# Optimization experiments

Measured on AMD Instinct MI355X. Metric: run time of the kernel, lower is better.

Reference implementation:

```python
import jax, jax.numpy as jnp
import numpy as np
from jax import lax

THRESH_WIDTH = 20  # default thresh_width in soft_skeletonize
SMOOTH = 1.0


def _max_pool3(x):
    # 3x3 max pool, stride 1, padding 1 (torch pads with -inf for max pool)
    return lax.reduce_window(x, -jnp.inf, lax.max,
                             (1, 1, 3, 3), (1, 1, 1, 1),
                             [(0, 0), (0, 0), (1, 1), (1, 1)])


def _soft_skeletonize(x):
    def body(i, x):
        min_pool_x = -_max_pool3(-x)
        contour = jax.nn.relu(_max_pool3(min_pool_x) - min_pool_x)
        return jax.nn.relu(x - contour)
    return lax.fori_loop(0, THRESH_WIDTH, body, x)


def _norm_intersection(center_line, vessel):
    clf = center_line.ravel()
    vf = vessel.ravel()
    intersection = jnp.sum(clf * vf)
    return (intersection + SMOOTH) / (jnp.sum(clf) + SMOOTH)


def setup_inputs() -> dict:
    key = jax.random.key(0)
    k1, k2 = jax.random.split(key)
    shape = (16, 1, 1024, 1024)
    pred = jax.random.uniform(k1, shape, dtype=jnp.float32)
    gt = jax.random.uniform(k2, shape, dtype=jnp.float32)
    return {"pred": pred, "gt": gt}


def reference(pred, gt):
    # channel == 1 path: pred used as-is (float)
    pred = pred.astype(jnp.float32)
    cl_pred = _soft_skeletonize(pred)
    target_skeleton = _soft_skeletonize(gt)
    iflat = _norm_intersection(cl_pred, gt)
    tflat = _norm_intersection(target_skeleton, pred)
    intersection = iflat * tflat
    loss = 1.0 - 2.0 * intersection / (iflat + tflat)
    return loss  # scalar; .squeeze() in torch is a no-op here
```

## Files before the change

kernel.cpp:

```cpp
#include <hip/hip_runtime.h>
#include <math.h>


#define IMG_H 1024
#define IMG_W 1024
#define IMG_N (IMG_H * IMG_W)
#define NIMG  16
#define NZ    32
#define BH    32
#define NBANDS (IMG_H / BH)
#define K     4
#define EW    258
#define NBLK  (NZ * NBANDS)
#define ITER_PAIRS ((BH + 6 * K) / 2)

typedef _Float16 h2 __attribute__((ext_vector_type(2)));

__device__ __forceinline__ h2 hmin2(h2 a, h2 b) { return __builtin_elementwise_min(a, b); }
__device__ __forceinline__ h2 hmax2(h2 a, h2 b) { return __builtin_elementwise_max(a, b); }

union U32H { unsigned u; h2 h; };
__device__ __forceinline__ unsigned as_u(h2 h) { U32H t; t.h = h; return t.u; }
__device__ __forceinline__ h2 as_h2(unsigned u) { U32H t; t.u = u; return t.h; }

struct Hp { h2 lo, hi; };
struct St { Hp hm1, hm2, m2, m3, q1, q2, x1, x2, x3, xc; };

template<int BUF>
__device__ __forceinline__ Hp stage_step(
    St& s, h2 rmask, int t, const uint2 (&e2)[2][EW])
{
    h2 lp = as_h2(e2[BUF][t].y);
    h2 rp = as_h2(e2[BUF][t + 2].x);
    h2 midx = (h2){s.xc.lo[1], s.xc.hi[0]};
    h2 hlo = hmin2(hmin2((h2){lp[0], s.xc.lo[0]}, s.xc.lo), midx);
    h2 hhi = hmin2(hmin2(midx, s.xc.hi), (h2){s.xc.hi[1], rp[0]});
    h2 mlo = hmin2(hmin2(hmin2(s.hm1.lo, s.hm2.lo), hlo), rmask);
    h2 mhi = hmin2(hmin2(hmin2(s.hm1.hi, s.hm2.hi), hhi), rmask);
    h2 midm = (h2){s.m2.lo[1], s.m2.hi[0]};
    h2 qlo = hmax2(hmax2((h2){lp[1], s.m2.lo[0]}, s.m2.lo), midm);
    h2 qhi = hmax2(hmax2(midm, s.m2.hi), (h2){s.m2.hi[1], rp[1]});
    h2 Mlo = hmax2(hmax2(s.q1.lo, s.q2.lo), qlo);
    h2 Mhi = hmax2(hmax2(s.q1.hi, s.q2.hi), qhi);
    const h2 Z2 = (h2){(_Float16)0.f, (_Float16)0.f};
    h2 elo = hmax2(s.x3.lo - hmax2(Mlo - s.m3.lo, Z2), Z2);
    h2 ehi = hmax2(s.x3.hi - hmax2(Mhi - s.m3.hi, Z2), Z2);
    s.hm1 = s.hm2; s.hm2.lo = hlo; s.hm2.hi = hhi;
    s.m3  = s.m2;  s.m2.lo  = mlo; s.m2.hi  = mhi;
    s.q1  = s.q2;  s.q2.lo  = qlo; s.q2.hi  = qhi;
    s.x3  = s.x2;  s.x2 = s.x1;    s.x1 = s.xc;
    Hp e; e.lo = elo; e.hi = ehi;
    return e;
}

template<int BUF, int FIRST, int LAST>
__device__ __forceinline__ void iter_step(
    int y, int t, int c, int r0, St (&st)[K],
    const float* __restrict__ f32src, const unsigned short* __restrict__ bsrc,
    unsigned short* __restrict__ bdst, const float* __restrict__ oth,
    float& a1, float& a2, uint2 (&e2)[K][2][EW])
{
    const _Float16 HINF = (_Float16)__builtin_huge_valf();
    const h2 PINF2 = (h2){HINF, HINF};
    const h2 NINF2 = (h2){-HINF, -HINF};

    Hp xnext; xnext.lo = PINF2; xnext.hi = PINF2;
    if ((unsigned)(y + 1) < (unsigned)IMG_H) {
        if constexpr (FIRST) {
            float4 f = *(const float4*)(f32src + (size_t)(y + 1) * IMG_W + c);
            xnext.lo = (h2){(_Float16)f.x, (_Float16)f.y};
            xnext.hi = (h2){(_Float16)f.z, (_Float16)f.w};
        } else {
            uint2 u = *(const uint2*)(bsrc + (size_t)(y + 1) * IMG_W + c);
            xnext.lo = as_h2(u.x);
            xnext.hi = as_h2(u.y);
        }
    }
    __syncthreads();

    h2 rm = ((unsigned)(y - 13) < (unsigned)IMG_H) ? PINF2 : NINF2;
    Hp eK = stage_step<BUF>(st[K - 1], rm, t, e2[K - 1]);
    #pragma unroll
    for (int k = K - 2; k >= 0; --k) {
        rm = ((unsigned)(y - 4 * k - 1) < (unsigned)IMG_H) ? PINF2 : NINF2;
        Hp e = stage_step<BUF>(st[k], rm, t, e2[k]);
        h2 em = ((unsigned)(y - 4 * k - 3) < (unsigned)IMG_H) ? NINF2 : PINF2;
        st[k + 1].xc.lo = hmax2(e.lo, em);
        st[k + 1].xc.hi = hmax2(e.hi, em);
    }
    st[0].xc = xnext;

    #pragma unroll
    for (int k = 0; k < K; ++k) {
        e2[k][BUF ^ 1][t + 1] = make_uint2(
            as_u((h2){st[k].xc.lo[0], st[k].m2.lo[0]}),
            as_u((h2){st[k].xc.hi[1], st[k].m2.hi[1]}));
    }

    int orow = y - (4 * (K - 1) + 3);
    if ((unsigned)(orow - r0) < (unsigned)BH) {
        if constexpr (!LAST) {
            *(uint2*)(bdst + (size_t)orow * IMG_W + c) =
                make_uint2(as_u(eK.lo), as_u(eK.hi));
        } else {
            float4 ov = *(const float4*)(oth + (size_t)orow * IMG_W + c);
            float e0 = (float)eK.lo[0], e1 = (float)eK.lo[1];
            float e2f = (float)eK.hi[0], e3 = (float)eK.hi[1];
            a1 += e0 * ov.x + e1 * ov.y + e2f * ov.z + e3 * ov.w;
            a2 += e0 + e1 + e2f + e3;
        }
    }
}

template<int FIRST, int LAST>
__global__ __launch_bounds__(256, 2) void skel(
    const unsigned short* __restrict__ src, unsigned short* __restrict__ dst,
    const float* __restrict__ pred32, const float* __restrict__ gt32,
    double* __restrict__ partials)
{
    __shared__ uint2 e2[K][2][EW];
    __shared__ double l1[4], l2[4];

    const int t = threadIdx.x, c = 4 * t;
    const int band = blockIdx.x, z = blockIdx.y;
    const int r0 = band * BH;
    const _Float16 HINF = (_Float16)__builtin_huge_valf();
    const h2 PINF2 = (h2){HINF, HINF};
    const h2 NINF2 = (h2){-HINF, -HINF};

    const float* f32src = (z < NIMG) ? pred32 + (size_t)z * IMG_N
                                     : gt32 + (size_t)(z - NIMG) * IMG_N;
    const unsigned short* bsrc = FIRST ? nullptr : src + (size_t)z * IMG_N;
    unsigned short* bdst = LAST ? nullptr : dst + (size_t)z * IMG_N;
    const float* oth = LAST ? ((z < NIMG) ? gt32 + (size_t)z * IMG_N
                                          : pred32 + (size_t)(z - NIMG) * IMG_N)
                            : nullptr;

    if (t < K) {
        #pragma unroll
        for (int b = 0; b < 2; ++b) {
            e2[t][b][0]      = make_uint2(0u, 0xFC007C00u);
            e2[t][b][EW - 1] = make_uint2(0xFC007C00u, 0u);
        }
    }

    St st[K];
    #pragma unroll
    for (int k = 0; k < K; ++k) {
        st[k].hm1.lo = st[k].hm1.hi = PINF2;
        st[k].hm2.lo = st[k].hm2.hi = PINF2;
        st[k].m2.lo  = st[k].m2.hi  = NINF2;
        st[k].m3.lo  = st[k].m3.hi  = NINF2;
        st[k].q1.lo  = st[k].q1.hi  = NINF2;
        st[k].q2.lo  = st[k].q2.hi  = NINF2;
        st[k].x1.lo  = st[k].x1.hi  = PINF2;
        st[k].x2.lo  = st[k].x2.hi  = PINF2;
        st[k].x3.lo  = st[k].x3.hi  = PINF2;
        st[k].xc.lo  = st[k].xc.hi  = PINF2;
    }

    const int y0 = r0 - 2 * K;
    if ((unsigned)y0 < (unsigned)IMG_H) {
        if constexpr (FIRST) {
            float4 f = *(const float4*)(f32src + (size_t)y0 * IMG_W + c);
            st[0].xc.lo = (h2){(_Float16)f.x, (_Float16)f.y};
            st[0].xc.hi = (h2){(_Float16)f.z, (_Float16)f.w};
        } else {
            uint2 u = *(const uint2*)(bsrc + (size_t)y0 * IMG_W + c);
            st[0].xc.lo = as_h2(u.x);
            st[0].xc.hi = as_h2(u.y);
        }
    }

    #pragma unroll
    for (int k = 0; k < K; ++k) {
        e2[k][0][t + 1] = make_uint2(
            as_u((h2){st[k].xc.lo[0], st[k].m2.lo[0]}),
            as_u((h2){st[k].xc.hi[1], st[k].m2.hi[1]}));
    }

    float a1 = 0.f, a2 = 0.f;
    for (int p = 0; p < ITER_PAIRS; ++p) {
        int y = y0 + 2 * p;
        iter_step<0, FIRST, LAST>(y,     t, c, r0, st, f32src, bsrc, bdst, oth, a1, a2, e2);
        iter_step<1, FIRST, LAST>(y + 1, t, c, r0, st, f32src, bsrc, bdst, oth, a1, a2, e2);
    }

    if constexpr (LAST) {
        double d1 = a1, d2 = a2;
        for (int off = 32; off; off >>= 1) {
            d1 += __shfl_down(d1, off);
            d2 += __shfl_down(d2, off);
        }
        const int w = t >> 6;
        if ((t & 63) == 0) { l1[w] = d1; l2[w] = d2; }
        __syncthreads();
        if (t == 0) {
            int bid = z * NBANDS + band;
            partials[2 * bid]     = l1[0] + l1[1] + l1[2] + l1[3];
            partials[2 * bid + 1] = l2[0] + l2[1] + l2[2] + l2[3];
        }
    }
}

__global__ __launch_bounds__(256) void finalize(
    const double* __restrict__ pp, float* __restrict__ out)
{
    __shared__ double sh[4][4];
    double i1 = 0, i2 = 0, t1 = 0, t2 = 0;
    for (int i = threadIdx.x; i < NBLK; i += 256) {
        double a = pp[2 * i], b = pp[2 * i + 1];
        if (i < NIMG * NBANDS) { i1 += a; i2 += b; }
        else                   { t1 += a; t2 += b; }
    }
    for (int off = 32; off; off >>= 1) {
        i1 += __shfl_down(i1, off); i2 += __shfl_down(i2, off);
        t1 += __shfl_down(t1, off); t2 += __shfl_down(t2, off);
    }
    const int w = threadIdx.x >> 6;
    if ((threadIdx.x & 63) == 0) { sh[0][w] = i1; sh[1][w] = i2; sh[2][w] = t1; sh[3][w] = t2; }
    __syncthreads();
    if (threadIdx.x == 0) {
        double s1 = 0, s2 = 0, s3 = 0, s4 = 0;
        for (int j = 0; j < 4; ++j) { s1 += sh[0][j]; s2 += sh[1][j]; s3 += sh[2][j]; s4 += sh[3][j]; }
        double iflat = (s1 + 1.0) / (s2 + 1.0);
        double tflat = (s3 + 1.0) / (s4 + 1.0);
        out[0] = (float)(1.0 - 2.0 * (iflat * tflat) / (iflat + tflat));
    }
}

extern "C" void kernel_launch(void* const* d_in, const int* in_sizes, int n_in,
                              void* d_out, int out_size, void* d_ws, size_t ws_size,
                              hipStream_t stream)
{
    const float* pred = (const float*)d_in[0];
    const float* gt   = (const float*)d_in[1];

    unsigned short* A = (unsigned short*)d_ws;
    unsigned short* B = A + (size_t)NZ * IMG_N;
    double* partials  = (double*)d_ws;
    dim3 grid(NBANDS, NZ);

    skel<1, 0><<<grid, 256, 0, stream>>>(nullptr, A, pred, gt, nullptr);
    skel<0, 0><<<grid, 256, 0, stream>>>(A, B, pred, gt, nullptr);
    skel<0, 0><<<grid, 256, 0, stream>>>(B, A, pred, gt, nullptr);
    skel<0, 0><<<grid, 256, 0, stream>>>(A, B, pred, gt, nullptr);
    skel<0, 1><<<grid, 256, 0, stream>>>(B, nullptr, pred, gt, partials);

    finalize<<<1, 256, 0, stream>>>(partials, (float*)d_out);
}
```

Baseline: 644.0 us.

## Fuse five skeleton iterations per pass and specialize interior bands without masks

```diff
diff --git a/kernel.cpp b/kernel.cpp
--- a/kernel.cpp
+++ b/kernel.cpp
@@ -9,7 +9,7 @@
 #define NZ    32
 #define BH    32
 #define NBANDS (IMG_H / BH)
-#define K     4
+#define K     5
 #define EW    258
 #define NBLK  (NZ * NBANDS)
 #define ITER_PAIRS ((BH + 6 * K) / 2)
@@ -23,20 +23,26 @@
 __device__ __forceinline__ unsigned as_u(h2 h) { U32H t; t.h = h; return t.u; }
 __device__ __forceinline__ h2 as_h2(unsigned u) { U32H t; t.u = u; return t.h; }
 
+#define HINF  ((_Float16)__builtin_huge_valf())
+#define PINF2 ((h2){HINF, HINF})
+#define NINF2 ((h2){-HINF, -HINF})
+
 struct Hp { h2 lo, hi; };
 struct St { Hp hm1, hm2, m2, m3, q1, q2, x1, x2, x3, xc; };
 
-template<int BUF>
+template<int BUF, bool MASK>
 __device__ __forceinline__ Hp stage_step(
-    St& s, h2 rmask, int t, const uint2 (&e2)[2][EW])
-{
-    h2 lp = as_h2(e2[BUF][t].y);
-    h2 rp = as_h2(e2[BUF][t + 2].x);
+    St& s, h2 rmask, int t,
+    const unsigned (&eX)[2][EW], const unsigned (&eY)[2][EW])
+{
+    h2 lp = as_h2(eY[BUF][t]);
+    h2 rp = as_h2(eX[BUF][t + 2]);
     h2 midx = (h2){s.xc.lo[1], s.xc.hi[0]};
     h2 hlo = hmin2(hmin2((h2){lp[0], s.xc.lo[0]}, s.xc.lo), midx);
     h2 hhi = hmin2(hmin2(midx, s.xc.hi), (h2){s.xc.hi[1], rp[0]});
-    h2 mlo = hmin2(hmin2(hmin2(s.hm1.lo, s.hm2.lo), hlo), rmask);
-    h2 mhi = hmin2(hmin2(hmin2(s.hm1.hi, s.hm2.hi), hhi), rmask);
+    h2 mlo = hmin2(hmin2(s.hm1.lo, s.hm2.lo), hlo);
+    h2 mhi = hmin2(hmin2(s.hm1.hi, s.hm2.hi), hhi);
+    if constexpr (MASK) { mlo = hmin2(mlo, rmask); mhi = hmin2(mhi, rmask); }
     h2 midm = (h2){s.m2.lo[1], s.m2.hi[0]};
     h2 qlo = hmax2(hmax2((h2){lp[1], s.m2.lo[0]}, s.m2.lo), midm);
     h2 qhi = hmax2(hmax2(midm, s.m2.hi), (h2){s.m2.hi[1], rp[1]});
@@ -53,48 +59,62 @@
     return e;
 }
 
-template<int BUF, int FIRST, int LAST>
+template<int BUF, bool MASK, int FIRST, int LAST>
 __device__ __forceinline__ void iter_step(
     int y, int t, int c, int r0, St (&st)[K],
     const float* __restrict__ f32src, const unsigned short* __restrict__ bsrc,
     unsigned short* __restrict__ bdst, const float* __restrict__ oth,
-    float& a1, float& a2, uint2 (&e2)[K][2][EW])
-{
-    const _Float16 HINF = (_Float16)__builtin_huge_valf();
-    const h2 PINF2 = (h2){HINF, HINF};
-    const h2 NINF2 = (h2){-HINF, -HINF};
-
-    Hp xnext; xnext.lo = PINF2; xnext.hi = PINF2;
-    if ((unsigned)(y + 1) < (unsigned)IMG_H) {
+    float& a1, float& a2,
+    unsigned (&eX)[K][2][EW], unsigned (&eY)[K][2][EW])
+{
+    Hp xnext;
+    if constexpr (MASK) {
+        xnext.lo = PINF2; xnext.hi = PINF2;
+        if ((unsigned)(y + 1) < (unsigned)IMG_H) {
+            if constexpr (FIRST) {
+                float4 f = *(const float4*)(f32src + (size_t)(y + 1) * IMG_W + c);
+                xnext.lo = (h2){(_Float16)f.x, (_Float16)f.y};
+                xnext.hi = (h2){(_Float16)f.z, (_Float16)f.w};
+            } else {
+                uint2 u = *(const uint2*)(bsrc + (size_t)(y + 1) * IMG_W + c);
+                xnext.lo = as_h2(u.x); xnext.hi = as_h2(u.y);
+            }
+        }
+    } else {
         if constexpr (FIRST) {
             float4 f = *(const float4*)(f32src + (size_t)(y + 1) * IMG_W + c);
             xnext.lo = (h2){(_Float16)f.x, (_Float16)f.y};
             xnext.hi = (h2){(_Float16)f.z, (_Float16)f.w};
         } else {
             uint2 u = *(const uint2*)(bsrc + (size_t)(y + 1) * IMG_W + c);
-            xnext.lo = as_h2(u.x);
-            xnext.hi = as_h2(u.y);
+            xnext.lo = as_h2(u.x); xnext.hi = as_h2(u.y);
         }
     }
     __syncthreads();
 
-    h2 rm = ((unsigned)(y - 13) < (unsigned)IMG_H) ? PINF2 : NINF2;
-    Hp eK = stage_step<BUF>(st[K - 1], rm, t, e2[K - 1]);
+    h2 rm = PINF2;
+    if constexpr (MASK)
+        rm = ((unsigned)(y - 4 * (K - 1) - 1) < (unsigned)IMG_H) ? PINF2 : NINF2;
+    Hp eK = stage_step<BUF, MASK>(st[K - 1], rm, t, eX[K - 1], eY[K - 1]);
     #pragma unroll
     for (int k = K - 2; k >= 0; --k) {
-        rm = ((unsigned)(y - 4 * k - 1) < (unsigned)IMG_H) ? PINF2 : NINF2;
-        Hp e = stage_step<BUF>(st[k], rm, t, e2[k]);
-        h2 em = ((unsigned)(y - 4 * k - 3) < (unsigned)IMG_H) ? NINF2 : PINF2;
-        st[k + 1].xc.lo = hmax2(e.lo, em);
-        st[k + 1].xc.hi = hmax2(e.hi, em);
+        if constexpr (MASK)
+            rm = ((unsigned)(y - 4 * k - 1) < (unsigned)IMG_H) ? PINF2 : NINF2;
+        Hp e = stage_step<BUF, MASK>(st[k], rm, t, eX[k], eY[k]);
+        if constexpr (MASK) {
+            h2 em = ((unsigned)(y - 4 * k - 3) < (unsigned)IMG_H) ? NINF2 : PINF2;
+            st[k + 1].xc.lo = hmax2(e.lo, em);
+            st[k + 1].xc.hi = hmax2(e.hi, em);
+        } else {
+            st[k + 1].xc = e;
+        }
     }
     st[0].xc = xnext;
 
     #pragma unroll
     for (int k = 0; k < K; ++k) {
-        e2[k][BUF ^ 1][t + 1] = make_uint2(
-            as_u((h2){st[k].xc.lo[0], st[k].m2.lo[0]}),
-            as_u((h2){st[k].xc.hi[1], st[k].m2.hi[1]}));
+        eX[k][BUF ^ 1][t + 1] = as_u((h2){st[k].xc.lo[0], st[k].m2.lo[0]});
+        eY[k][BUF ^ 1][t + 1] = as_u((h2){st[k].xc.hi[1], st[k].m2.hi[1]});
     }
 
     int orow = y - (4 * (K - 1) + 3);
@@ -112,21 +132,34 @@
     }
 }
 
+template<bool MASK, int FIRST, int LAST>
+__device__ __forceinline__ void run_band(
+    int y0, int t, int c, int r0, St (&st)[K],
+    const float* __restrict__ f32src, const unsigned short* __restrict__ bsrc,
+    unsigned short* __restrict__ bdst, const float* __restrict__ oth,
+    float& a1, float& a2,
+    unsigned (&eX)[K][2][EW], unsigned (&eY)[K][2][EW])
+{
+    for (int p = 0; p < ITER_PAIRS; ++p) {
+        int y = y0 + 2 * p;
+        iter_step<0, MASK, FIRST, LAST>(y,     t, c, r0, st, f32src, bsrc, bdst, oth, a1, a2, eX, eY);
+        iter_step<1, MASK, FIRST, LAST>(y + 1, t, c, r0, st, f32src, bsrc, bdst, oth, a1, a2, eX, eY);
+    }
+}
+
 template<int FIRST, int LAST>
 __global__ __launch_bounds__(256, 2) void skel(
     const unsigned short* __restrict__ src, unsigned short* __restrict__ dst,
     const float* __restrict__ pred32, const float* __restrict__ gt32,
     double* __restrict__ partials)
 {
-    __shared__ uint2 e2[K][2][EW];
+    __shared__ unsigned eX[K][2][EW];
+    __shared__ unsigned eY[K][2][EW];
     __shared__ double l1[4], l2[4];
 
     const int t = threadIdx.x, c = 4 * t;
     const int band = blockIdx.x, z = blockIdx.y;
     const int r0 = band * BH;
-    const _Float16 HINF = (_Float16)__builtin_huge_valf();
-    const h2 PINF2 = (h2){HINF, HINF};
-    const h2 NINF2 = (h2){-HINF, -HINF};
 
     const float* f32src = (z < NIMG) ? pred32 + (size_t)z * IMG_N
                                      : gt32 + (size_t)(z - NIMG) * IMG_N;
@@ -139,8 +172,8 @@
     if (t < K) {
         #pragma unroll
         for (int b = 0; b < 2; ++b) {
-            e2[t][b][0]      = make_uint2(0u, 0xFC007C00u);
-            e2[t][b][EW - 1] = make_uint2(0xFC007C00u, 0u);
+            eY[t][b][0]      = 0xFC007C00u;
+            eX[t][b][EW - 1] = 0xFC007C00u;
         }
     }
 
@@ -167,24 +200,21 @@
             st[0].xc.hi = (h2){(_Float16)f.z, (_Float16)f.w};
         } else {
             uint2 u = *(const uint2*)(bsrc + (size_t)y0 * IMG_W + c);
-            st[0].xc.lo = as_h2(u.x);
-            st[0].xc.hi = as_h2(u.y);
+            st[0].xc.lo = as_h2(u.x); st[0].xc.hi = as_h2(u.y);
         }
     }
 
     #pragma unroll
     for (int k = 0; k < K; ++k) {
-        e2[k][0][t + 1] = make_uint2(
-            as_u((h2){st[k].xc.lo[0], st[k].m2.lo[0]}),
-            as_u((h2){st[k].xc.hi[1], st[k].m2.hi[1]}));
+        eX[k][0][t + 1] = as_u((h2){st[k].xc.lo[0], st[k].m2.lo[0]});
+        eY[k][0][t + 1] = as_u((h2){st[k].xc.hi[1], st[k].m2.hi[1]});
     }
 
     float a1 = 0.f, a2 = 0.f;
-    for (int p = 0; p < ITER_PAIRS; ++p) {
-        int y = y0 + 2 * p;
-        iter_step<0, FIRST, LAST>(y,     t, c, r0, st, f32src, bsrc, bdst, oth, a1, a2, e2);
-        iter_step<1, FIRST, LAST>(y + 1, t, c, r0, st, f32src, bsrc, bdst, oth, a1, a2, e2);
-    }
+    if (band >= 1 && band <= NBANDS - 2)
+        run_band<false, FIRST, LAST>(y0, t, c, r0, st, f32src, bsrc, bdst, oth, a1, a2, eX, eY);
+    else
+        run_band<true,  FIRST, LAST>(y0, t, c, r0, st, f32src, bsrc, bdst, oth, a1, a2, eX, eY);
 
     if constexpr (LAST) {
         double d1 = a1, d2 = a2;
@@ -238,14 +268,13 @@
 
     unsigned short* A = (unsigned short*)d_ws;
     unsigned short* B = A + (size_t)NZ * IMG_N;
-    double* partials  = (double*)d_ws;
+    double* partials  = (double*)B;
     dim3 grid(NBANDS, NZ);
 
     skel<1, 0><<<grid, 256, 0, stream>>>(nullptr, A, pred, gt, nullptr);
     skel<0, 0><<<grid, 256, 0, stream>>>(A, B, pred, gt, nullptr);
     skel<0, 0><<<grid, 256, 0, stream>>>(B, A, pred, gt, nullptr);
-    skel<0, 0><<<grid, 256, 0, stream>>>(A, B, pred, gt, nullptr);
-    skel<0, 1><<<grid, 256, 0, stream>>>(B, nullptr, pred, gt, partials);
+    skel<0, 1><<<grid, 256, 0, stream>>>(A, nullptr, pred, gt, partials);
 
     finalize<<<1, 256, 0, stream>>>(partials, (float*)d_out);
 }
```

After: 711.2 us. +10.4%, slower.

## Process two rows per pipeline step to halve barriers and share vertical windows

Applied to the files above, without the earlier changes.

```diff
diff --git a/kernel.cpp b/kernel.cpp
--- a/kernel.cpp
+++ b/kernel.cpp
@@ -12,7 +12,7 @@
 #define K     4
 #define EW    258
 #define NBLK  (NZ * NBANDS)
-#define ITER_PAIRS ((BH + 6 * K) / 2)
+#define NPAIR 16
 
 typedef _Float16 h2 __attribute__((ext_vector_type(2)));
 
@@ -23,34 +23,64 @@
 __device__ __forceinline__ unsigned as_u(h2 h) { U32H t; t.h = h; return t.u; }
 __device__ __forceinline__ h2 as_h2(unsigned u) { U32H t; t.u = u; return t.h; }
 
+#define PXP 0x7C007C00u
+#define NXP 0xFC00FC00u
+#define HINF  ((_Float16)__builtin_huge_valf())
+#define PINF2 ((h2){HINF, HINF})
+#define NINF2 ((h2){-HINF, -HINF})
+
 struct Hp { h2 lo, hi; };
-struct St { Hp hm1, hm2, m2, m3, q1, q2, x1, x2, x3, xc; };
+
+struct St { Hp hm1, hm2, mpa, mpb, mppb, qpa, qpb, xpa, xpb, xppa, xppb, xca, xcb; };
 
 template<int BUF>
-__device__ __forceinline__ Hp stage_step(
-    St& s, h2 rmask, int t, const uint2 (&e2)[2][EW])
-{
-    h2 lp = as_h2(e2[BUF][t].y);
-    h2 rp = as_h2(e2[BUF][t + 2].x);
-    h2 midx = (h2){s.xc.lo[1], s.xc.hi[0]};
-    h2 hlo = hmin2(hmin2((h2){lp[0], s.xc.lo[0]}, s.xc.lo), midx);
-    h2 hhi = hmin2(hmin2(midx, s.xc.hi), (h2){s.xc.hi[1], rp[0]});
-    h2 mlo = hmin2(hmin2(hmin2(s.hm1.lo, s.hm2.lo), hlo), rmask);
-    h2 mhi = hmin2(hmin2(hmin2(s.hm1.hi, s.hm2.hi), hhi), rmask);
-    h2 midm = (h2){s.m2.lo[1], s.m2.hi[0]};
-    h2 qlo = hmax2(hmax2((h2){lp[1], s.m2.lo[0]}, s.m2.lo), midm);
-    h2 qhi = hmax2(hmax2(midm, s.m2.hi), (h2){s.m2.hi[1], rp[1]});
-    h2 Mlo = hmax2(hmax2(s.q1.lo, s.q2.lo), qlo);
-    h2 Mhi = hmax2(hmax2(s.q1.hi, s.q2.hi), qhi);
+__device__ __forceinline__ void stage_step(
+    St& s, int ya, int t,
+    const uint2 (&eXk)[2][EW], const uint2 (&eYk)[2][EW],
+    Hp& ea, Hp& eb)
+{
     const h2 Z2 = (h2){(_Float16)0.f, (_Float16)0.f};
-    h2 elo = hmax2(s.x3.lo - hmax2(Mlo - s.m3.lo, Z2), Z2);
-    h2 ehi = hmax2(s.x3.hi - hmax2(Mhi - s.m3.hi, Z2), Z2);
-    s.hm1 = s.hm2; s.hm2.lo = hlo; s.hm2.hi = hhi;
-    s.m3  = s.m2;  s.m2.lo  = mlo; s.m2.hi  = mhi;
-    s.q1  = s.q2;  s.q2.lo  = qlo; s.q2.hi  = qhi;
-    s.x3  = s.x2;  s.x2 = s.x1;    s.x1 = s.xc;
-    Hp e; e.lo = elo; e.hi = ehi;
-    return e;
+    uint2 lp = eYk[BUF][t];
+    uint2 rp = eXk[BUF][t + 2];
+    h2 lpx = as_h2(lp.x), lpm = as_h2(lp.y);
+    h2 rpx = as_h2(rp.x), rpm = as_h2(rp.y);
+
+    h2 midA = (h2){s.xca.lo[1], s.xca.hi[0]};
+    h2 haLo = hmin2(hmin2((h2){lpx[0], s.xca.lo[0]}, s.xca.lo), midA);
+    h2 haHi = hmin2(hmin2(midA, s.xca.hi), (h2){s.xca.hi[1], rpx[0]});
+    h2 midB = (h2){s.xcb.lo[1], s.xcb.hi[0]};
+    h2 hbLo = hmin2(hmin2((h2){lpx[1], s.xcb.lo[0]}, s.xcb.lo), midB);
+    h2 hbHi = hmin2(hmin2(midB, s.xcb.hi), (h2){s.xcb.hi[1], rpx[1]});
+
+    h2 rmA = as_h2(((unsigned)(ya - 1) < (unsigned)IMG_H) ? PXP : NXP);
+    h2 rmB = as_h2(((unsigned)(ya)     < (unsigned)IMG_H) ? PXP : NXP);
+    h2 maLo = hmin2(hmin2(hmin2(s.hm1.lo, s.hm2.lo), haLo), rmA);
+    h2 maHi = hmin2(hmin2(hmin2(s.hm1.hi, s.hm2.hi), haHi), rmA);
+    h2 mbLo = hmin2(hmin2(hmin2(s.hm2.lo, haLo), hbLo), rmB);
+    h2 mbHi = hmin2(hmin2(hmin2(s.hm2.hi, haHi), hbHi), rmB);
+
+    h2 midQa = (h2){s.mpa.lo[1], s.mpa.hi[0]};
+    h2 qaLo = hmax2(hmax2((h2){lpm[0], s.mpa.lo[0]}, s.mpa.lo), midQa);
+    h2 qaHi = hmax2(hmax2(midQa, s.mpa.hi), (h2){s.mpa.hi[1], rpm[0]});
+    h2 midQb = (h2){s.mpb.lo[1], s.mpb.hi[0]};
+    h2 qbLo = hmax2(hmax2((h2){lpm[1], s.mpb.lo[0]}, s.mpb.lo), midQb);
+    h2 qbHi = hmax2(hmax2(midQb, s.mpb.hi), (h2){s.mpb.hi[1], rpm[1]});
+
+    h2 MaLo = hmax2(hmax2(s.qpa.lo, s.qpb.lo), qaLo);
+    h2 MaHi = hmax2(hmax2(s.qpa.hi, s.qpb.hi), qaHi);
+    h2 MbLo = hmax2(hmax2(s.qpb.lo, qaLo), qbLo);
+    h2 MbHi = hmax2(hmax2(s.qpb.hi, qaHi), qbHi);
+
+    ea.lo = hmax2(s.xppa.lo - hmax2(MaLo - s.mppb.lo, Z2), Z2);
+    ea.hi = hmax2(s.xppa.hi - hmax2(MaHi - s.mppb.hi, Z2), Z2);
+    eb.lo = hmax2(s.xppb.lo - hmax2(MbLo - s.mpa.lo, Z2), Z2);
+    eb.hi = hmax2(s.xppb.hi - hmax2(MbHi - s.mpa.hi, Z2), Z2);
+
+    s.hm1.lo = haLo; s.hm1.hi = haHi; s.hm2.lo = hbLo; s.hm2.hi = hbHi;
+    s.mppb = s.mpb;
+    s.mpa.lo = maLo; s.mpa.hi = maHi; s.mpb.lo = mbLo; s.mpb.hi = mbHi;
+    s.qpa.lo = qaLo; s.qpa.hi = qaHi; s.qpb.lo = qbLo; s.qpb.hi = qbHi;
+    s.xppa = s.xpa; s.xppb = s.xpb; s.xpa = s.xca; s.xpb = s.xcb;
 }
 
 template<int BUF, int FIRST, int LAST>
@@ -58,57 +88,78 @@
     int y, int t, int c, int r0, St (&st)[K],
     const float* __restrict__ f32src, const unsigned short* __restrict__ bsrc,
     unsigned short* __restrict__ bdst, const float* __restrict__ oth,
-    float& a1, float& a2, uint2 (&e2)[K][2][EW])
-{
-    const _Float16 HINF = (_Float16)__builtin_huge_valf();
-    const h2 PINF2 = (h2){HINF, HINF};
-    const h2 NINF2 = (h2){-HINF, -HINF};
-
-    Hp xnext; xnext.lo = PINF2; xnext.hi = PINF2;
-    if ((unsigned)(y + 1) < (unsigned)IMG_H) {
-        if constexpr (FIRST) {
-            float4 f = *(const float4*)(f32src + (size_t)(y + 1) * IMG_W + c);
-            xnext.lo = (h2){(_Float16)f.x, (_Float16)f.y};
-            xnext.hi = (h2){(_Float16)f.z, (_Float16)f.w};
+    float& a1, float& a2,
+    uint2 (&eX)[K][2][EW], uint2 (&eY)[K][2][EW])
+{
+    int la = y + 2; la = la < 0 ? 0 : (la > IMG_H - 1 ? IMG_H - 1 : la);
+    int lb = y + 3; lb = lb < 0 ? 0 : (lb > IMG_H - 1 ? IMG_H - 1 : lb);
+    h2 gA = as_h2(((unsigned)(y + 2) < (unsigned)IMG_H) ? NXP : PXP);
+    h2 gB = as_h2(((unsigned)(y + 3) < (unsigned)IMG_H) ? NXP : PXP);
+    Hp xna, xnb;
+    if constexpr (FIRST) {
+        float4 fa = *(const float4*)(f32src + (size_t)la * IMG_W + c);
+        float4 fb = *(const float4*)(f32src + (size_t)lb * IMG_W + c);
+        xna.lo = (h2){(_Float16)fa.x, (_Float16)fa.y};
+        xna.hi = (h2){(_Float16)fa.z, (_Float16)fa.w};
+        xnb.lo = (h2){(_Float16)fb.x, (_Float16)fb.y};
+        xnb.hi = (h2){(_Float16)fb.z, (_Float16)fb.w};
+    } else {
+        uint2 ua = *(const uint2*)(bsrc + (size_t)la * IMG_W + c);
+        uint2 ub = *(const uint2*)(bsrc + (size_t)lb * IMG_W + c);
+        xna.lo = as_h2(ua.x); xna.hi = as_h2(ua.y);
+        xnb.lo = as_h2(ub.x); xnb.hi = as_h2(ub.y);
+    }
+    xna.lo = hmax2(xna.lo, gA); xna.hi = hmax2(xna.hi, gA);
+    xnb.lo = hmax2(xnb.lo, gB); xnb.hi = hmax2(xnb.hi, gB);
+
+    __syncthreads();
+
+    Hp ea, eb;
+    stage_step<BUF>(st[K - 1], y - 6 * (K - 1), t, eX[K - 1], eY[K - 1], ea, eb);
+    int orow = y - 6 * (K - 1) - 4;
+    if ((unsigned)(orow - r0) < (unsigned)BH) {
+        if constexpr (!LAST) {
+            *(uint2*)(bdst + (size_t)orow * IMG_W + c) = make_uint2(as_u(ea.lo), as_u(ea.hi));
         } else {
-            uint2 u = *(const uint2*)(bsrc + (size_t)(y + 1) * IMG_W + c);
-            xnext.lo = as_h2(u.x);
-            xnext.hi = as_h2(u.y);
-        }
-    }
-    __syncthreads();
-
-    h2 rm = ((unsigned)(y - 13) < (unsigned)IMG_H) ? PINF2 : NINF2;
-    Hp eK = stage_step<BUF>(st[K - 1], rm, t, e2[K - 1]);
+            float4 ov = *(const float4*)(oth + (size_t)orow * IMG_W + c);
+            float e0 = (float)ea.lo[0], e1 = (float)ea.lo[1];
+            float e2 = (float)ea.hi[0], e3 = (float)ea.hi[1];
+            a1 += e0 * ov.x + e1 * ov.y + e2 * ov.z + e3 * ov.w;
+            a2 += e0 + e1 + e2 + e3;
+        }
+    }
+    if ((unsigned)(orow + 1 - r0) < (unsigned)BH) {
+        if constexpr (!LAST) {
+            *(uint2*)(bdst + (size_t)(orow + 1) * IMG_W + c) = make_uint2(as_u(eb.lo), as_u(eb.hi));
+        } else {
+            float4 ov = *(const float4*)(oth + (size_t)(orow + 1) * IMG_W + c);
+            float e0 = (float)eb.lo[0], e1 = (float)eb.lo[1];
+            float e2 = (float)eb.hi[0], e3 = (float)eb.hi[1];
+            a1 += e0 * ov.x + e1 * ov.y + e2 * ov.z + e3 * ov.w;
+            a2 += e0 + e1 + e2 + e3;
+        }
+    }
+
     #pragma unroll
     for (int k = K - 2; k >= 0; --k) {
-        rm = ((unsigned)(y - 4 * k - 1) < (unsigned)IMG_H) ? PINF2 : NINF2;
-        Hp e = stage_step<BUF>(st[k], rm, t, e2[k]);
-        h2 em = ((unsigned)(y - 4 * k - 3) < (unsigned)IMG_H) ? NINF2 : PINF2;
-        st[k + 1].xc.lo = hmax2(e.lo, em);
-        st[k + 1].xc.hi = hmax2(e.hi, em);
-    }
-    st[0].xc = xnext;
+        Hp fa, fb;
+        int ya = y - 6 * k;
+        stage_step<BUF>(st[k], ya, t, eX[k], eY[k], fa, fb);
+        h2 eA = as_h2(((unsigned)(ya - 4) < (unsigned)IMG_H) ? NXP : PXP);
+        h2 eB = as_h2(((unsigned)(ya - 3) < (unsigned)IMG_H) ? NXP : PXP);
+        st[k + 1].xca.lo = hmax2(fa.lo, eA); st[k + 1].xca.hi = hmax2(fa.hi, eA);
+        st[k + 1].xcb.lo = hmax2(fb.lo, eB); st[k + 1].xcb.hi = hmax2(fb.hi, eB);
+    }
+    st[0].xca = xna; st[0].xcb = xnb;
 
     #pragma unroll
     for (int k = 0; k < K; ++k) {
-        e2[k][BUF ^ 1][t + 1] = make_uint2(
-            as_u((h2){st[k].xc.lo[0], st[k].m2.lo[0]}),
-            as_u((h2){st[k].xc.hi[1], st[k].m2.hi[1]}));
-    }
-
-    int orow = y - (4 * (K - 1) + 3);
-    if ((unsigned)(orow - r0) < (unsigned)BH) {
-        if constexpr (!LAST) {
-            *(uint2*)(bdst + (size_t)orow * IMG_W + c) =
-                make_uint2(as_u(eK.lo), as_u(eK.hi));
-        } else {
-            float4 ov = *(const float4*)(oth + (size_t)orow * IMG_W + c);
-            float e0 = (float)eK.lo[0], e1 = (float)eK.lo[1];
-            float e2f = (float)eK.hi[0], e3 = (float)eK.hi[1];
-            a1 += e0 * ov.x + e1 * ov.y + e2f * ov.z + e3 * ov.w;
-            a2 += e0 + e1 + e2f + e3;
-        }
+        eX[k][BUF ^ 1][t + 1] = make_uint2(
+            as_u((h2){st[k].xca.lo[0], st[k].xcb.lo[0]}),
+            as_u((h2){st[k].mpa.lo[0], st[k].mpb.lo[0]}));
+        eY[k][BUF ^ 1][t + 1] = make_uint2(
+            as_u((h2){st[k].xca.hi[1], st[k].xcb.hi[1]}),
+            as_u((h2){st[k].mpa.hi[1], st[k].mpb.hi[1]}));
     }
 }
 
@@ -118,15 +169,13 @@
     const float* __restrict__ pred32, const float* __restrict__ gt32,
     double* __restrict__ partials)
 {
-    __shared__ uint2 e2[K][2][EW];
+    __shared__ uint2 eX[K][2][EW];
+    __shared__ uint2 eY[K][2][EW];
     __shared__ double l1[4], l2[4];
 
     const int t = threadIdx.x, c = 4 * t;
     const int band = blockIdx.x, z = blockIdx.y;
     const int r0 = band * BH;
-    const _Float16 HINF = (_Float16)__builtin_huge_valf();
-    const h2 PINF2 = (h2){HINF, HINF};
-    const h2 NINF2 = (h2){-HINF, -HINF};
 
     const float* f32src = (z < NIMG) ? pred32 + (size_t)z * IMG_N
                                      : gt32 + (size_t)(z - NIMG) * IMG_N;
@@ -139,8 +188,8 @@
     if (t < K) {
         #pragma unroll
         for (int b = 0; b < 2; ++b) {
-            e2[t][b][0]      = make_uint2(0u, 0xFC007C00u);
-            e2[t][b][EW - 1] = make_uint2(0xFC007C00u, 0u);
+            eY[t][b][0]      = make_uint2(PXP, NXP);
+            eX[t][b][EW - 1] = make_uint2(PXP, NXP);
         }
     }
 
@@ -149,41 +198,57 @@
     for (int k = 0; k < K; ++k) {
         st[k].hm1.lo = st[k].hm1.hi = PINF2;
         st[k].hm2.lo = st[k].hm2.hi = PINF2;
-        st[k].m2.lo  = st[k].m2.hi  = NINF2;
-        st[k].m3.lo  = st[k].m3.hi  = NINF2;
-        st[k].q1.lo  = st[k].q1.hi  = NINF2;
-        st[k].q2.lo  = st[k].q2.hi  = NINF2;
-        st[k].x1.lo  = st[k].x1.hi  = PINF2;
-        st[k].x2.lo  = st[k].x2.hi  = PINF2;
-        st[k].x3.lo  = st[k].x3.hi  = PINF2;
-        st[k].xc.lo  = st[k].xc.hi  = PINF2;
-    }
-
-    const int y0 = r0 - 2 * K;
-    if ((unsigned)y0 < (unsigned)IMG_H) {
+        st[k].mpa.lo = st[k].mpa.hi = NINF2;
+        st[k].mpb.lo = st[k].mpb.hi = NINF2;
+        st[k].mppb.lo = st[k].mppb.hi = NINF2;
+        st[k].qpa.lo = st[k].qpa.hi = NINF2;
+        st[k].qpb.lo = st[k].qpb.hi = NINF2;
+        st[k].xpa.lo = st[k].xpa.hi = PINF2;
+        st[k].xpb.lo = st[k].xpb.hi = PINF2;
+        st[k].xppa.lo = st[k].xppa.hi = PINF2;
+        st[k].xppb.lo = st[k].xppb.hi = PINF2;
+        st[k].xca.lo = st[k].xca.hi = PINF2;
+        st[k].xcb.lo = st[k].xcb.hi = PINF2;
+    }
+
+    const int y0 = r0 - 8;
+    {
+        int la = y0 < 0 ? 0 : y0;
+        int lb = y0 + 1 < 0 ? 0 : y0 + 1;
+        h2 gA = as_h2(((unsigned)y0 < (unsigned)IMG_H) ? NXP : PXP);
+        h2 gB = as_h2(((unsigned)(y0 + 1) < (unsigned)IMG_H) ? NXP : PXP);
         if constexpr (FIRST) {
-            float4 f = *(const float4*)(f32src + (size_t)y0 * IMG_W + c);
-            st[0].xc.lo = (h2){(_Float16)f.x, (_Float16)f.y};
-            st[0].xc.hi = (h2){(_Float16)f.z, (_Float16)f.w};
+            float4 fa = *(const float4*)(f32src + (size_t)la * IMG_W + c);
+            float4 fb = *(const float4*)(f32src + (size_t)lb * IMG_W + c);
+            st[0].xca.lo = hmax2((h2){(_Float16)fa.x, (_Float16)fa.y}, gA);
+            st[0].xca.hi = hmax2((h2){(_Float16)fa.z, (_Float16)fa.w}, gA);
+            st[0].xcb.lo = hmax2((h2){(_Float16)fb.x, (_Float16)fb.y}, gB);
+            st[0].xcb.hi = hmax2((h2){(_Float16)fb.z, (_Float16)fb.w}, gB);
         } else {
-            uint2 u = *(const uint2*)(bsrc + (size_t)y0 * IMG_W + c);
-            st[0].xc.lo = as_h2(u.x);
-            st[0].xc.hi = as_h2(u.y);
+            uint2 ua = *(const uint2*)(bsrc + (size_t)la * IMG_W + c);
+            uint2 ub = *(const uint2*)(bsrc + (size_t)lb * IMG_W + c);
+            st[0].xca.lo = hmax2(as_h2(ua.x), gA);
+            st[0].xca.hi = hmax2(as_h2(ua.y), gA);
+            st[0].xcb.lo = hmax2(as_h2(ub.x), gB);
+            st[0].xcb.hi = hmax2(as_h2(ub.y), gB);
         }
     }
 
     #pragma unroll
     for (int k = 0; k < K; ++k) {
-        e2[k][0][t + 1] = make_uint2(
-            as_u((h2){st[k].xc.lo[0], st[k].m2.lo[0]}),
-            as_u((h2){st[k].xc.hi[1], st[k].m2.hi[1]}));
+        eX[k][0][t + 1] = make_uint2(
+            as_u((h2){st[k].xca.lo[0], st[k].xcb.lo[0]}),
+            as_u((h2){st[k].mpa.lo[0], st[k].mpb.lo[0]}));
+        eY[k][0][t + 1] = make_uint2(
+            as_u((h2){st[k].xca.hi[1], st[k].xcb.hi[1]}),
+            as_u((h2){st[k].mpa.hi[1], st[k].mpb.hi[1]}));
     }
 
     float a1 = 0.f, a2 = 0.f;
-    for (int p = 0; p < ITER_PAIRS; ++p) {
-        int y = y0 + 2 * p;
-        iter_step<0, FIRST, LAST>(y,     t, c, r0, st, f32src, bsrc, bdst, oth, a1, a2, e2);
-        iter_step<1, FIRST, LAST>(y + 1, t, c, r0, st, f32src, bsrc, bdst, oth, a1, a2, e2);
+    for (int p = 0; p < NPAIR; ++p) {
+        int y = y0 + 4 * p;
+        iter_step<0, FIRST, LAST>(y,     t, c, r0, st, f32src, bsrc, bdst, oth, a1, a2, eX, eY);
+        iter_step<1, FIRST, LAST>(y + 2, t, c, r0, st, f32src, bsrc, bdst, oth, a1, a2, eX, eY);
     }
 
     if constexpr (LAST) {
```

New measurement: 674.9 us. 4.8% more time.
